# Performance work log

Hardware: AMD Instinct MI355X
Metric: run time of the kernel (lower is better)

The kernel has to match this reference:

```python
import jax, jax.numpy as jnp
import numpy as np

B, HW, N = 32, 4096, 16
E, KV, FFN = 256, 256, 1024
NUM_ITER = 3
EPS_LN = 1e-5
EPS_ATTN = 1e-5


def _ln(x, g, b):
    m = x.mean(-1, keepdims=True)
    v = ((x - m) ** 2).mean(-1, keepdims=True)
    return (x - m) / jnp.sqrt(v + EPS_LN) * g + b


def _gru_cell(x, h, w_ih, w_hh, b_ih, b_hh):
    # PyTorch GRUCell semantics; gate order r, z, n
    gi = x @ w_ih.T + b_ih
    gh = h @ w_hh.T + b_hh
    ir, iz, inn = jnp.split(gi, 3, axis=-1)
    hr, hz, hn = jnp.split(gh, 3, axis=-1)
    r = jax.nn.sigmoid(ir + hr)
    z = jax.nn.sigmoid(iz + hz)
    n = jnp.tanh(inn + r * hn)
    return (1.0 - z) * n + z * h


def setup_inputs() -> dict:
    key = jax.random.key(0)
    ks = jax.random.split(key, 16)
    s = 0.02
    return {
        "input": jax.random.normal(ks[0], (B, HW, KV), jnp.float32),
        "query": jax.random.normal(ks[1], (B, N, E), jnp.float32),
        "g_kv": jnp.ones((KV,), jnp.float32),
        "b_kv": jnp.zeros((KV,), jnp.float32),
        "w_k": jax.random.normal(ks[2], (E, KV), jnp.float32) * s,
        "w_v": jax.random.normal(ks[3], (E, KV), jnp.float32) * s,
        "g_q": jnp.ones((E,), jnp.float32),
        "b_q": jnp.zeros((E,), jnp.float32),
        "w_q": jax.random.normal(ks[4], (E, E), jnp.float32) * s,
        "w_ih": jax.random.normal(ks[5], (3 * E, E), jnp.float32) * s,
        "w_hh": jax.random.normal(ks[6], (3 * E, E), jnp.float32) * s,
        "b_ih": jnp.zeros((3 * E,), jnp.float32),
        "b_hh": jnp.zeros((3 * E,), jnp.float32),
        "g_2": jnp.ones((E,), jnp.float32),
        "b_2": jnp.zeros((E,), jnp.float32),
        "w_f1": jax.random.normal(ks[7], (FFN, E), jnp.float32) * s,
        "b_f1": jnp.zeros((FFN,), jnp.float32),
        "w_f2": jax.random.normal(ks[8], (E, FFN), jnp.float32) * s,
        "b_f2": jnp.zeros((E,), jnp.float32),
    }


def reference(input, query, g_kv, b_kv, w_k, w_v, g_q, b_q, w_q,
              w_ih, w_hh, b_ih, b_hh, g_2, b_2, w_f1, b_f1, w_f2, b_f2):
    b, n, e = query.shape
    kv = _ln(input, g_kv, b_kv)              # (b, hw, kv)
    k = kv @ w_k.T                           # (b, hw, e)
    v = kv @ w_v.T                           # (b, hw, e)
    scale = e ** (-0.5)

    q = query
    attn = None
    for i in range(NUM_ITER):
        if i + 1 == NUM_ITER:  # bi-level truncated backprop
            q = jax.lax.stop_gradient(q) + query - jax.lax.stop_gradient(query)
        slots_prev = q
        qn = _ln(q, g_q, b_q)
        qp = (qn @ w_q.T) * scale            # (b, n, e)
        logit = jnp.einsum("bqc,bkc->bqk", qp, k)
        attn = jax.nn.softmax(logit, axis=1)           # softmax over slots (inverted)
        attn_w = attn / (attn.sum(2, keepdims=True) + EPS_ATTN)
        updates = jnp.einsum("bqk,bkc->bqc", attn_w, v)
        slots = _gru_cell(updates.reshape(b * n, e), slots_prev.reshape(b * n, e),
                          w_ih, w_hh, b_ih, b_hh).reshape(b, n, e)
        h = jax.nn.gelu(_ln(slots, g_2, b_2) @ w_f1.T + b_f1)
        q = slots + h @ w_f2.T + b_f2
    return q, attn
```

## Files before the change

### kernel.cpp

```cpp
#include <hip/hip_runtime.h>
#include <math.h>

#define NB 32
#define HW 4096
#define NS 16
#define EDIM 256
#define FFND 1024
#define EPS_LN 1e-5f
#define EPS_ATTN 1e-5f
#define BPB 32
#define RPB 128
#define TROWS 16

__device__ __forceinline__ float sigmoidf_(float x) { return 1.0f / (1.0f + __expf(-x)); }
__device__ __forceinline__ float gelu_(float x) {
    float x3 = x * x * x;
    return 0.5f * x * (1.0f + tanhf(0.7978845608028654f * (x + 0.044715f * x3)));
}

__device__ __forceinline__ float rsum16(float v) {
    int x;
    x = __builtin_amdgcn_update_dpp(0, __float_as_int(v), 0x128, 0xF, 0xF, true);
    v += __int_as_float(x);
    x = __builtin_amdgcn_update_dpp(0, __float_as_int(v), 0x124, 0xF, 0xF, true);
    v += __int_as_float(x);
    x = __builtin_amdgcn_update_dpp(0, __float_as_int(v), 0x122, 0xF, 0xF, true);
    v += __int_as_float(x);
    x = __builtin_amdgcn_update_dpp(0, __float_as_int(v), 0x121, 0xF, 0xF, true);
    v += __int_as_float(x);
    return v;
}

__global__ void k_prep(const float* __restrict__ w_q, const float* __restrict__ w_k,
                       float* __restrict__ W) {
    const int j = blockIdx.x;
    const int c = threadIdx.x;
    float acc = 0.f;
    for (int e = 0; e < EDIM; ++e)
        acc += w_q[e * EDIM + j] * w_k[e * EDIM + c];
    W[j * EDIM + c] = acc * 0.0625f;
}

__global__ __launch_bounds__(256) void k_tr(const float* __restrict__ src,
                                            float* __restrict__ dst, int R, int C) {
    __shared__ float tile[64][65];
    const int tilesC = C >> 6;
    const int tR = (blockIdx.x / tilesC) << 6;
    const int tC = (blockIdx.x % tilesC) << 6;
    const int t = threadIdx.x;
    {
        const int r = t >> 2;
        const int c0 = (t & 3) << 4;
#pragma unroll
        for (int i = 0; i < 16; i += 4) {
            const float4 v = *reinterpret_cast<const float4*>(src + (size_t)(tR + r) * C + tC + c0 + i);
            tile[r][c0 + i] = v.x; tile[r][c0 + i + 1] = v.y;
            tile[r][c0 + i + 2] = v.z; tile[r][c0 + i + 3] = v.w;
        }
    }
    __syncthreads();
    {
        const int c = t >> 2;
        const int r0 = (t & 3) << 4;
#pragma unroll
        for (int i = 0; i < 16; ++i)
            dst[(size_t)(tC + c) * R + tR + r0 + i] = tile[r0 + i][c];
    }
}

__global__ void k_qproj(const float* __restrict__ qsrc, const float* __restrict__ g_q,
                        const float* __restrict__ b_q, const float* __restrict__ W,
                        const float* __restrict__ g_kv, const float* __restrict__ b_kv,
                        float* __restrict__ qpk, float* __restrict__ gqbq) {
    const int row = blockIdx.x;
    const int t = threadIdx.x;
    __shared__ float qn[EDIM];
    __shared__ float red[16];
    const float v = qsrc[(size_t)row * EDIM + t];
    float s = v, ss = v * v;
#pragma unroll
    for (int m = 1; m < 64; m <<= 1) { s += __shfl_xor(s, m); ss += __shfl_xor(ss, m); }
    const int wave = t >> 6, lane = t & 63;
    if (lane == 0) { red[wave] = s; red[8 + wave] = ss; }
    __syncthreads();
    const float st = red[0] + red[1] + red[2] + red[3];
    const float sst = red[8] + red[9] + red[10] + red[11];
    const float mean = st * (1.0f / EDIM);
    const float rstd = rsqrtf(sst * (1.0f / EDIM) - mean * mean + EPS_LN);
    qn[t] = (v - mean) * rstd * g_q[t] + b_q[t];
    __syncthreads();
    float acc = 0.f;
    for (int j = 0; j < EDIM; ++j)
        acc += qn[j] * W[j * EDIM + t];
    qpk[(size_t)row * EDIM + t] = acc;
    float u = acc * g_kv[t];
    float w2 = acc * b_kv[t];
#pragma unroll
    for (int m = 1; m < 64; m <<= 1) { u += __shfl_xor(u, m); w2 += __shfl_xor(w2, m); }
    __syncthreads();
    if (lane == 0) { red[wave] = u; red[8 + wave] = w2; }
    __syncthreads();
    if (t == 0) {
        const int b = row >> 4, sl = row & 15;
        gqbq[b * 32 + sl] = red[0] + red[1] + red[2] + red[3];
        gqbq[b * 32 + 16 + sl] = red[8] + red[9] + red[10] + red[11];
    }
}

template <bool LAST>
__global__ __launch_bounds__(256, 2) void k_bigpass(
    const float* __restrict__ input, const float* __restrict__ qpk,
    const float* __restrict__ gqbq, const float* __restrict__ g_kv,
    float* __restrict__ pacc, float* __restrict__ psum, float* __restrict__ attn_out) {
    const int b = blockIdx.x >> 5;
    const int sub = blockIdx.x & 31;
    const int t = threadIdx.x;
    const int w = t >> 6;
    const int lane = t & 63;
    const int g = t >> 4;
    const int j = t & 15;

    __shared__ __align__(16) float G[NS][EDIM];
    __shared__ __align__(16) float stage[TROWS][264];
    __shared__ __align__(16) float wrec[TROWS][20];
    __shared__ float gqbq_s[2][NS];

#pragma unroll
    for (int i = 0; i < 4; ++i) {
        const int idx = i * 1024 + t * 4;
        const float4 qv = *reinterpret_cast<const float4*>(qpk + (size_t)b * 4096 + idx);
        const float4 gv = *reinterpret_cast<const float4*>(g_kv + (idx & 255));
        *reinterpret_cast<float4*>(&G[0][0] + idx) =
            make_float4(qv.x * gv.x, qv.y * gv.y, qv.z * gv.z, qv.w * gv.w);
    }
    if (t < 32) gqbq_s[t >> 4][t & 15] = gqbq[b * 32 + t];
    __syncthreads();

    float acc[4][4];
    float S[4], A[4];
#pragma unroll
    for (int si = 0; si < 4; ++si) {
        acc[si][0] = acc[si][1] = acc[si][2] = acc[si][3] = 0.f;
        S[si] = 0.f; A[si] = 0.f;
    }

    const int rowbase = sub * RPB;
#pragma unroll 1
    for (int tt = 0; tt < RPB / TROWS; ++tt) {
        const int grow = rowbase + tt * TROWS + g;
        const float* xa = input + ((size_t)b * HW + grow) * EDIM;

        float p[NS];
#pragma unroll
        for (int s = 0; s < NS; ++s) p[s] = 0.f;
        float s1 = 0.f, s2 = 0.f;
#pragma unroll
        for (int c = 0; c < 4; ++c) {
            const int off = (c * 16 + j) * 4;
            const float4 x = *reinterpret_cast<const float4*>(xa + off);
            *reinterpret_cast<float4*>(&stage[g][off]) = x;
            s1 += x.x + x.y + x.z + x.w;
            s2 += x.x * x.x + x.y * x.y + x.z * x.z + x.w * x.w;
#pragma unroll
            for (int s = 0; s < NS; ++s) {
                const float4 gg = *reinterpret_cast<const float4*>(&G[s][off]);
                p[s] += x.x * gg.x + x.y * gg.y + x.z * gg.z + x.w * gg.w;
            }
        }
        s1 = rsum16(s1);
        s2 = rsum16(s2);
#pragma unroll
        for (int s = 0; s < NS; ++s) p[s] = rsum16(p[s]);

        const float mean = s1 * (1.0f / EDIM);
        const float rstd = rsqrtf(s2 * (1.0f / EDIM) - mean * mean + EPS_LN);
        float mx = -1e30f;
#pragma unroll
        for (int s = 0; s < NS; ++s) {
            p[s] = rstd * (p[s] - mean * gqbq_s[0][s]) + gqbq_s[1][s];
            mx = fmaxf(mx, p[s]);
        }
        float tot = 0.f;
#pragma unroll
        for (int s = 0; s < NS; ++s) { p[s] = __expf(p[s] - mx); tot += p[s]; }
        const float inv = 1.0f / tot;
#pragma unroll
        for (int s = 0; s < NS; ++s) p[s] *= inv;

        if (j == 0) {
#pragma unroll
            for (int sq = 0; sq < 4; ++sq)
                *reinterpret_cast<float4*>(&wrec[g][sq * 4]) =
                    make_float4(p[sq * 4], p[sq * 4 + 1], p[sq * 4 + 2], p[sq * 4 + 3]);
            wrec[g][16] = rstd;
            wrec[g][17] = rstd * mean;
            if (LAST) {
#pragma unroll
                for (int s = 0; s < NS; ++s)
                    attn_out[((size_t)(b * NS + s)) * HW + grow] = p[s];
            }
        }
        __syncthreads();

        {
            const int ch = lane * 4;
            const int sbase = w * 4;
#pragma unroll
            for (int r = 0; r < TROWS; ++r) {
                const float4 xv = *reinterpret_cast<const float4*>(&stage[r][ch]);
                const float4 at = *reinterpret_cast<const float4*>(&wrec[r][sbase]);
                const float rr = wrec[r][16];
                const float rm = wrec[r][17];
                float wg;
                wg = at.x * rr;
                acc[0][0] += wg * xv.x; acc[0][1] += wg * xv.y;
                acc[0][2] += wg * xv.z; acc[0][3] += wg * xv.w;
                S[0] += at.x; A[0] += at.x * rm;
                wg = at.y * rr;
                acc[1][0] += wg * xv.x; acc[1][1] += wg * xv.y;
                acc[1][2] += wg * xv.z; acc[1][3] += wg * xv.w;
                S[1] += at.y; A[1] += at.y * rm;
                wg = at.z * rr;
                acc[2][0] += wg * xv.x; acc[2][1] += wg * xv.y;
                acc[2][2] += wg * xv.z; acc[2][3] += wg * xv.w;
                S[2] += at.z; A[2] += at.z * rm;
                wg = at.w * rr;
                acc[3][0] += wg * xv.x; acc[3][1] += wg * xv.y;
                acc[3][2] += wg * xv.z; acc[3][3] += wg * xv.w;
                S[3] += at.w; A[3] += at.w * rm;
            }
        }
        __syncthreads();
    }

#pragma unroll
    for (int si = 0; si < 4; ++si) {
        *reinterpret_cast<float4*>(
            pacc + ((size_t)blockIdx.x * NS + w * 4 + si) * EDIM + lane * 4) =
            make_float4(acc[si][0], acc[si][1], acc[si][2], acc[si][3]);
    }
    if (lane == 0) {
#pragma unroll
        for (int si = 0; si < 4; ++si) {
            psum[blockIdx.x * 32 + w * 4 + si] = S[si];
            psum[blockIdx.x * 32 + 16 + w * 4 + si] = A[si];
        }
    }
}

__global__ __launch_bounds__(256) void k_upd(
    const float* __restrict__ pacc, const float* __restrict__ psum,
    const float* __restrict__ g_kv, const float* __restrict__ b_kv,
    const float* __restrict__ w_vT, float* __restrict__ updates) {
    const int rt = blockIdx.x >> 1;
    const int ct = blockIdx.x & 1;
    const int row0 = rt * 4;
    const int b = row0 >> 4;
    const int s0 = row0 & 15;
    const int t = threadIdx.x;
    __shared__ __align__(16) float ub[4][EDIM];
    __shared__ float sSA[4][2];

    if (t < 8) {
        const int r = t & 3;
        const int isA = t >> 2;
        float v = 0.f;
        for (int p = 0; p < BPB; ++p)
            v += psum[(b * BPB + p) * 32 + isA * 16 + s0 + r];
        sSA[r][isA] = v;
    }
    __syncthreads();
#pragma unroll
    for (int r = 0; r < 4; ++r) {
        float V = 0.f;
        for (int p = 0; p < BPB; ++p)
            V += pacc[((size_t)(b * BPB + p) * NS + s0 + r) * EDIM + t];
        const float Sv = sSA[r][0], Av = sSA[r][1];
        ub[r][t] = (g_kv[t] * (V - Av) + b_kv[t] * Sv) / (Sv + EPS_ATTN);
    }
    __syncthreads();

    const int c = ct * 128 + (t & 127);
    const int half = t >> 7;
    const float* u0 = ub[2 * half];
    const float* u1 = ub[2 * half + 1];
    float a0 = 0.f, a1 = 0.f;
#pragma unroll 4
    for (int j = 0; j < EDIM; j += 4) {
        const float4 x0 = *reinterpret_cast<const float4*>(u0 + j);
        const float4 x1 = *reinterpret_cast<const float4*>(u1 + j);
        const float w0 = w_vT[(size_t)j * EDIM + c];
        const float w1 = w_vT[(size_t)(j + 1) * EDIM + c];
        const float w2 = w_vT[(size_t)(j + 2) * EDIM + c];
        const float w3 = w_vT[(size_t)(j + 3) * EDIM + c];
        a0 += x0.x * w0 + x0.y * w1 + x0.z * w2 + x0.w * w3;
        a1 += x1.x * w0 + x1.y * w1 + x1.z * w2 + x1.w * w3;
    }
    updates[(size_t)(row0 + 2 * half) * EDIM + c] = a0;
    updates[(size_t)(row0 + 2 * half + 1) * EDIM + c] = a1;
}

__global__ __launch_bounds__(256) void k_gates(
    const float* __restrict__ updates, const float* __restrict__ qprev,
    const float* __restrict__ w_ihT, const float* __restrict__ w_hhT,
    const float* __restrict__ b_ih, const float* __restrict__ b_hh,
    float* __restrict__ gig) {
    const int rt = blockIdx.x / 6;
    const int ct = blockIdx.x % 6;
    const int row0 = rt * 4;
    const int t = threadIdx.x;
    const bool ih = ct < 3;
    const int lc = (ih ? ct : ct - 3) * 256 + t;
    const float* __restrict__ src = ih ? updates : qprev;
    const float* __restrict__ wT = ih ? w_ihT : w_hhT;

    __shared__ __align__(16) float in4[4][EDIM];
#pragma unroll
    for (int r = 0; r < 4; ++r)
        in4[r][t] = src[(size_t)(row0 + r) * EDIM + t];
    __syncthreads();

    float a0 = 0.f, a1 = 0.f, a2 = 0.f, a3 = 0.f;
#pragma unroll 4
    for (int j = 0; j < EDIM; j += 4) {
        const float4 x0 = *reinterpret_cast<const float4*>(&in4[0][j]);
        const float4 x1 = *reinterpret_cast<const float4*>(&in4[1][j]);
        const float4 x2 = *reinterpret_cast<const float4*>(&in4[2][j]);
        const float4 x3 = *reinterpret_cast<const float4*>(&in4[3][j]);
        const float w0 = wT[(size_t)j * 768 + lc];
        const float w1 = wT[(size_t)(j + 1) * 768 + lc];
        const float w2 = wT[(size_t)(j + 2) * 768 + lc];
        const float w3 = wT[(size_t)(j + 3) * 768 + lc];
        a0 += x0.x * w0 + x0.y * w1 + x0.z * w2 + x0.w * w3;
        a1 += x1.x * w0 + x1.y * w1 + x1.z * w2 + x1.w * w3;
        a2 += x2.x * w0 + x2.y * w1 + x2.z * w2 + x2.w * w3;
        a3 += x3.x * w0 + x3.y * w1 + x3.z * w2 + x3.w * w3;
    }
    const float bias = ih ? b_ih[lc] : b_hh[lc];
    const int gcol = ih ? lc : 768 + lc;
    gig[(size_t)(row0 + 0) * 1536 + gcol] = a0 + bias;
    gig[(size_t)(row0 + 1) * 1536 + gcol] = a1 + bias;
    gig[(size_t)(row0 + 2) * 1536 + gcol] = a2 + bias;
    gig[(size_t)(row0 + 3) * 1536 + gcol] = a3 + bias;
}

__global__ __launch_bounds__(256) void k_gruffn1(
    const float* __restrict__ gig, const float* __restrict__ qprev,
    const float* __restrict__ g_2, const float* __restrict__ b_2,
    const float* __restrict__ w_f1T, const float* __restrict__ b_f1,
    float* __restrict__ slots, float* __restrict__ h1) {
    const int rt = blockIdx.x >> 2;
    const int ct = blockIdx.x & 3;
    const int row0 = rt * 4;
    const int t = threadIdx.x;
    const int wave = t >> 6, lane = t & 63;
    __shared__ __align__(16) float ln2[4][EDIM];
    __shared__ float red[4][8];

    float sl[4];
#pragma unroll
    for (int r = 0; r < 4; ++r) {
        const size_t base = (size_t)(row0 + r) * 1536;
        const float ir = gig[base + t];
        const float iz = gig[base + 256 + t];
        const float inn = gig[base + 512 + t];
        const float hr = gig[base + 768 + t];
        const float hz = gig[base + 1024 + t];
        const float hn = gig[base + 1280 + t];
        const float h = qprev[(size_t)(row0 + r) * EDIM + t];
        const float rg = sigmoidf_(ir + hr);
        const float z = sigmoidf_(iz + hz);
        const float n = tanhf(inn + rg * hn);
        sl[r] = (1.0f - z) * n + z * h;
    }
    if (ct == 0) {
#pragma unroll
        for (int r = 0; r < 4; ++r)
            slots[(size_t)(row0 + r) * EDIM + t] = sl[r];
    }
    {
        float a[4], qq[4];
#pragma unroll
        for (int r = 0; r < 4; ++r) { a[r] = sl[r]; qq[r] = sl[r] * sl[r]; }
#pragma unroll
        for (int m = 1; m < 64; m <<= 1) {
#pragma unroll
            for (int r = 0; r < 4; ++r) {
                a[r] += __shfl_xor(a[r], m);
                qq[r] += __shfl_xor(qq[r], m);
            }
        }
        if (lane == 0) {
#pragma unroll
            for (int r = 0; r < 4; ++r) { red[wave][r] = a[r]; red[wave][4 + r] = qq[r]; }
        }
    }
    __syncthreads();
    {
        const float g = g_2[t], bb = b_2[t];
#pragma unroll
        for (int r = 0; r < 4; ++r) {
            const float Sv = red[0][r] + red[1][r] + red[2][r] + red[3][r];
            const float Qv = red[0][4 + r] + red[1][4 + r] + red[2][4 + r] + red[3][4 + r];
            const float mn = Sv * (1.0f / EDIM);
            const float rs = rsqrtf(Qv * (1.0f / EDIM) - mn * mn + EPS_LN);
            ln2[r][t] = (sl[r] - mn) * rs * g + bb;
        }
    }
    __syncthreads();

    const int c = ct * 256 + t;
    float a0 = 0.f, a1 = 0.f, a2 = 0.f, a3 = 0.f;
#pragma unroll 4
    for (int j = 0; j < EDIM; j += 4) {
        const float4 x0 = *reinterpret_cast<const float4*>(&ln2[0][j]);
        const float4 x1 = *reinterpret_cast<const float4*>(&ln2[1][j]);
        const float4 x2 = *reinterpret_cast<const float4*>(&ln2[2][j]);
        const float4 x3 = *reinterpret_cast<const float4*>(&ln2[3][j]);
        const float w0 = w_f1T[(size_t)j * FFND + c];
        const float w1 = w_f1T[(size_t)(j + 1) * FFND + c];
        const float w2 = w_f1T[(size_t)(j + 2) * FFND + c];
        const float w3 = w_f1T[(size_t)(j + 3) * FFND + c];
        a0 += x0.x * w0 + x0.y * w1 + x0.z * w2 + x0.w * w3;
        a1 += x1.x * w0 + x1.y * w1 + x1.z * w2 + x1.w * w3;
        a2 += x2.x * w0 + x2.y * w1 + x2.z * w2 + x2.w * w3;
        a3 += x3.x * w0 + x3.y * w1 + x3.z * w2 + x3.w * w3;
    }
    const float bf = b_f1[c];
    h1[(size_t)(row0 + 0) * FFND + c] = gelu_(a0 + bf);
    h1[(size_t)(row0 + 1) * FFND + c] = gelu_(a1 + bf);
    h1[(size_t)(row0 + 2) * FFND + c] = gelu_(a2 + bf);
    h1[(size_t)(row0 + 3) * FFND + c] = gelu_(a3 + bf);
}

__global__ __launch_bounds__(256) void k_ffn2qpk(
    const float* __restrict__ h1, const float* __restrict__ slots,
    const float* __restrict__ w_f2T, const float* __restrict__ b_f2,
    const float* __restrict__ query,
    const float* __restrict__ g_q, const float* __restrict__ b_q,
    const float* __restrict__ W,
    const float* __restrict__ g_kv, const float* __restrict__ b_kv,
    float* __restrict__ q_out, float* __restrict__ qpk, float* __restrict__ gqbq,
    int adjust, int do_qpk) {
    const int row0 = blockIdx.x * 2;
    const int t = threadIdx.x;
    const int wave = t >> 6, lane = t & 63;
    __shared__ __align__(16) float in2[2][FFND];
    __shared__ float red[4][4];
    __shared__ __align__(16) float qn[2][EDIM];

#pragma unroll
    for (int r = 0; r < 2; ++r)
        *reinterpret_cast<float4*>(&in2[r][t * 4]) =
            *reinterpret_cast<const float4*>(h1 + (size_t)(row0 + r) * FFND + t * 4);
    __syncthreads();
    float a0 = 0.f, a1 = 0.f;
#pragma unroll 4
    for (int j = 0; j < FFND; j += 4) {
        const float4 x0 = *reinterpret_cast<const float4*>(&in2[0][j]);
        const float4 x1 = *reinterpret_cast<const float4*>(&in2[1][j]);
        const float w0 = w_f2T[(size_t)j * EDIM + t];
        const float w1 = w_f2T[(size_t)(j + 1) * EDIM + t];
        const float w2 = w_f2T[(size_t)(j + 2) * EDIM + t];
        const float w3 = w_f2T[(size_t)(j + 3) * EDIM + t];
        a0 += x0.x * w0 + x0.y * w1 + x0.z * w2 + x0.w * w3;
        a1 += x1.x * w0 + x1.y * w1 + x1.z * w2 + x1.w * w3;
    }
    const float bf = b_f2[t];
    float v0 = slots[(size_t)row0 * EDIM + t] + a0 + bf;
    float v1 = slots[(size_t)(row0 + 1) * EDIM + t] + a1 + bf;
    if (adjust) {
        const float qq0 = query[(size_t)row0 * EDIM + t];
        const float qq1 = query[(size_t)(row0 + 1) * EDIM + t];
        v0 = (v0 + qq0) - qq0;
        v1 = (v1 + qq1) - qq1;
    }
    q_out[(size_t)row0 * EDIM + t] = v0;
    q_out[(size_t)(row0 + 1) * EDIM + t] = v1;

    if (!do_qpk) return;

    {
        float a0r = v0, q0 = v0 * v0, a1r = v1, q1 = v1 * v1;
#pragma unroll
        for (int m = 1; m < 64; m <<= 1) {
            a0r += __shfl_xor(a0r, m); q0 += __shfl_xor(q0, m);
            a1r += __shfl_xor(a1r, m); q1 += __shfl_xor(q1, m);
        }
        if (lane == 0) { red[wave][0] = a0r; red[wave][1] = q0; red[wave][2] = a1r; red[wave][3] = q1; }
    }
    __syncthreads();
    {
        const float S0 = red[0][0] + red[1][0] + red[2][0] + red[3][0];
        const float Q0 = red[0][1] + red[1][1] + red[2][1] + red[3][1];
        const float S1 = red[0][2] + red[1][2] + red[2][2] + red[3][2];
        const float Q1 = red[0][3] + red[1][3] + red[2][3] + red[3][3];
        const float m0 = S0 * (1.0f / EDIM);
        const float r0 = rsqrtf(Q0 * (1.0f / EDIM) - m0 * m0 + EPS_LN);
        const float m1 = S1 * (1.0f / EDIM);
        const float r1 = rsqrtf(Q1 * (1.0f / EDIM) - m1 * m1 + EPS_LN);
        const float g = g_q[t], bb = b_q[t];
        qn[0][t] = (v0 - m0) * r0 * g + bb;
        qn[1][t] = (v1 - m1) * r1 * g + bb;
    }
    __syncthreads();
    float p0 = 0.f, p1 = 0.f;
#pragma unroll 4
    for (int j = 0; j < EDIM; j += 4) {
        const float4 x0 = *reinterpret_cast<const float4*>(&qn[0][j]);
        const float4 x1 = *reinterpret_cast<const float4*>(&qn[1][j]);
        const float w0 = W[(size_t)j * EDIM + t];
        const float w1 = W[(size_t)(j + 1) * EDIM + t];
        const float w2 = W[(size_t)(j + 2) * EDIM + t];
        const float w3 = W[(size_t)(j + 3) * EDIM + t];
        p0 += x0.x * w0 + x0.y * w1 + x0.z * w2 + x0.w * w3;
        p1 += x1.x * w0 + x1.y * w1 + x1.z * w2 + x1.w * w3;
    }
    qpk[(size_t)row0 * EDIM + t] = p0;
    qpk[(size_t)(row0 + 1) * EDIM + t] = p1;
    {
        const float gk = g_kv[t], bk = b_kv[t];
        float u0 = p0 * gk, w0 = p0 * bk, u1 = p1 * gk, w1 = p1 * bk;
#pragma unroll
        for (int m = 1; m < 64; m <<= 1) {
            u0 += __shfl_xor(u0, m); w0 += __shfl_xor(w0, m);
            u1 += __shfl_xor(u1, m); w1 += __shfl_xor(w1, m);
        }
        __syncthreads();
        if (lane == 0) { red[wave][0] = u0; red[wave][1] = w0; red[wave][2] = u1; red[wave][3] = w1; }
        __syncthreads();
        if (t == 0) {
            const int b = row0 >> 4;
            const int sl = row0 & 15;
            gqbq[b * 32 + sl] = red[0][0] + red[1][0] + red[2][0] + red[3][0];
            gqbq[b * 32 + 16 + sl] = red[0][1] + red[1][1] + red[2][1] + red[3][1];
            gqbq[b * 32 + sl + 1] = red[0][2] + red[1][2] + red[2][2] + red[3][2];
            gqbq[b * 32 + 16 + sl + 1] = red[0][3] + red[1][3] + red[2][3] + red[3][3];
        }
    }
}

extern "C" void kernel_launch(void* const* d_in, const int* in_sizes, int n_in,
                              void* d_out, int out_size, void* d_ws, size_t ws_size,
                              hipStream_t stream) {
    const float* input = (const float*)d_in[0];
    const float* query = (const float*)d_in[1];
    const float* g_kv = (const float*)d_in[2];
    const float* b_kv = (const float*)d_in[3];
    const float* w_k = (const float*)d_in[4];
    const float* w_v = (const float*)d_in[5];
    const float* g_q = (const float*)d_in[6];
    const float* b_q = (const float*)d_in[7];
    const float* w_q = (const float*)d_in[8];
    const float* w_ih = (const float*)d_in[9];
    const float* w_hh = (const float*)d_in[10];
    const float* b_ih = (const float*)d_in[11];
    const float* b_hh = (const float*)d_in[12];
    const float* g_2 = (const float*)d_in[13];
    const float* b_2 = (const float*)d_in[14];
    const float* w_f1 = (const float*)d_in[15];
    const float* b_f1 = (const float*)d_in[16];
    const float* w_f2 = (const float*)d_in[17];
    const float* b_f2 = (const float*)d_in[18];

    float* ws = (float*)d_ws;
    float* W = ws;        ws += 65536;
    float* qpk = ws;      ws += 131072;
    float* gqbq = ws;     ws += 1024;
    float* psum = ws;     ws += 32768;
    float* q_ws = ws;     ws += 131072;
    float* updates = ws;  ws += 131072;
    float* slots = ws;    ws += 131072;
    float* w_vT = ws;     ws += 65536;
    float* w_ihT = ws;    ws += 196608;
    float* w_hhT = ws;    ws += 196608;
    float* w_f1T = ws;    ws += 262144;
    float* w_f2T = ws;    ws += 262144;
    float* pacc = ws;     ws += (size_t)NB * BPB * NS * EDIM;
    float* gig = pacc;
    float* h1 = pacc + 786432;

    float* out_q = (float*)d_out;
    float* out_attn = out_q + (size_t)NB * NS * EDIM;

    k_prep<<<256, 256, 0, stream>>>(w_q, w_k, W);
    k_tr<<<16, 256, 0, stream>>>(w_v, w_vT, 256, 256);
    k_tr<<<48, 256, 0, stream>>>(w_ih, w_ihT, 768, 256);
    k_tr<<<48, 256, 0, stream>>>(w_hh, w_hhT, 768, 256);
    k_tr<<<64, 256, 0, stream>>>(w_f1, w_f1T, 1024, 256);
    k_tr<<<64, 256, 0, stream>>>(w_f2, w_f2T, 256, 1024);
    k_qproj<<<512, 256, 0, stream>>>(query, g_q, b_q, W, g_kv, b_kv, qpk, gqbq);

    const float* qprev[3] = {query, q_ws, q_ws};
    float* qdst[3] = {q_ws, q_ws, out_q};
    const int adj[3] = {0, 1, 0};

    for (int it = 0; it < 3; ++it) {
        const bool last = (it == 2);
        if (last)
            k_bigpass<true><<<NB * BPB, 256, 0, stream>>>(input, qpk, gqbq, g_kv, pacc, psum, out_attn);
        else
            k_bigpass<false><<<NB * BPB, 256, 0, stream>>>(input, qpk, gqbq, g_kv, pacc, psum, nullptr);
        k_upd<<<256, 256, 0, stream>>>(pacc, psum, g_kv, b_kv, w_vT, updates);
        k_gates<<<768, 256, 0, stream>>>(updates, qprev[it], w_ihT, w_hhT, b_ih, b_hh, gig);
        k_gruffn1<<<512, 256, 0, stream>>>(gig, qprev[it], g_2, b_2, w_f1T, b_f1, slots, h1);
        k_ffn2qpk<<<256, 256, 0, stream>>>(h1, slots, w_f2T, b_f2, query, g_q, b_q, W,
                                           g_kv, b_kv, qdst[it], qpk, gqbq,
                                           adj[it], last ? 0 : 1);
    }
}
```

Before: 495.7 us.

## Hold slot projections in registers and split logit work across waves

Each wave now keeps four slots' worth of the gamma-scaled query-key projection in registers instead of reading all 16 slots from shared memory for every row. The logit computation is split so each wave handles 4 slots across the staged rows, with results written to a small LDS table. The softmax over slots then runs with one slot per lane using DPP max and sum reductions, and the attention output is written by all 16 lanes rather than by one. This reduces LDS traffic and the per-thread 16-way reduction work, but adds two barriers per tile and 64 extra registers per thread for Greg, which may hurt occupancy under the 2-blocks launch bound.

```diff
diff --git a/kernel.cpp b/kernel.cpp
--- a/kernel.cpp
+++ b/kernel.cpp
@@ -30,6 +30,18 @@
     v += __int_as_float(x);
     return v;
 }
+__device__ __forceinline__ float rmax16(float v) {
+    int x;
+    x = __builtin_amdgcn_update_dpp(0, __float_as_int(v), 0x128, 0xF, 0xF, true);
+    v = fmaxf(v, __int_as_float(x));
+    x = __builtin_amdgcn_update_dpp(0, __float_as_int(v), 0x124, 0xF, 0xF, true);
+    v = fmaxf(v, __int_as_float(x));
+    x = __builtin_amdgcn_update_dpp(0, __float_as_int(v), 0x122, 0xF, 0xF, true);
+    v = fmaxf(v, __int_as_float(x));
+    x = __builtin_amdgcn_update_dpp(0, __float_as_int(v), 0x121, 0xF, 0xF, true);
+    v = fmaxf(v, __int_as_float(x));
+    return v;
+}
 
 __global__ void k_prep(const float* __restrict__ w_q, const float* __restrict__ w_k,
                        float* __restrict__ W) {
@@ -117,24 +129,29 @@
     const int t = threadIdx.x;
     const int w = t >> 6;
     const int lane = t & 63;
+    const int gp = (t >> 4) & 3;
     const int g = t >> 4;
     const int j = t & 15;
 
-    __shared__ __align__(16) float G[NS][EDIM];
     __shared__ __align__(16) float stage[TROWS][264];
     __shared__ __align__(16) float wrec[TROWS][20];
-    __shared__ float gqbq_s[2][NS];
-
-#pragma unroll
-    for (int i = 0; i < 4; ++i) {
-        const int idx = i * 1024 + t * 4;
-        const float4 qv = *reinterpret_cast<const float4*>(qpk + (size_t)b * 4096 + idx);
-        const float4 gv = *reinterpret_cast<const float4*>(g_kv + (idx & 255));
-        *reinterpret_cast<float4*>(&G[0][0] + idx) =
-            make_float4(qv.x * gv.x, qv.y * gv.y, qv.z * gv.z, qv.w * gv.w);
-    }
-    if (t < 32) gqbq_s[t >> 4][t & 15] = gqbq[b * 32 + t];
-    __syncthreads();
+    __shared__ __align__(16) float logit_lds[TROWS][NS];
+
+    const float gqj = gqbq[b * 32 + j];
+    const float bqj = gqbq[b * 32 + 16 + j];
+
+    float4 Greg[4][4];
+#pragma unroll
+    for (int sp = 0; sp < 4; ++sp) {
+#pragma unroll
+        for (int c = 0; c < 4; ++c) {
+            const int off = (c * 16 + j) * 4;
+            const float4 qv = *reinterpret_cast<const float4*>(
+                qpk + (size_t)b * 4096 + (w * 4 + sp) * 256 + off);
+            const float4 gv = *reinterpret_cast<const float4*>(g_kv + off);
+            Greg[sp][c] = make_float4(qv.x * gv.x, qv.y * gv.y, qv.z * gv.z, qv.w * gv.w);
+        }
+    }
 
     float acc[4][4];
     float S[4], A[4];
@@ -150,9 +167,6 @@
         const int grow = rowbase + tt * TROWS + g;
         const float* xa = input + ((size_t)b * HW + grow) * EDIM;
 
-        float p[NS];
-#pragma unroll
-        for (int s = 0; s < NS; ++s) p[s] = 0.f;
         float s1 = 0.f, s2 = 0.f;
 #pragma unroll
         for (int c = 0; c < 4; ++c) {
@@ -161,44 +175,47 @@
             *reinterpret_cast<float4*>(&stage[g][off]) = x;
             s1 += x.x + x.y + x.z + x.w;
             s2 += x.x * x.x + x.y * x.y + x.z * x.z + x.w * x.w;
-#pragma unroll
-            for (int s = 0; s < NS; ++s) {
-                const float4 gg = *reinterpret_cast<const float4*>(&G[s][off]);
-                p[s] += x.x * gg.x + x.y * gg.y + x.z * gg.z + x.w * gg.w;
-            }
         }
         s1 = rsum16(s1);
         s2 = rsum16(s2);
-#pragma unroll
-        for (int s = 0; s < NS; ++s) p[s] = rsum16(p[s]);
-
         const float mean = s1 * (1.0f / EDIM);
         const float rstd = rsqrtf(s2 * (1.0f / EDIM) - mean * mean + EPS_LN);
-        float mx = -1e30f;
-#pragma unroll
-        for (int s = 0; s < NS; ++s) {
-            p[s] = rstd * (p[s] - mean * gqbq_s[0][s]) + gqbq_s[1][s];
-            mx = fmaxf(mx, p[s]);
-        }
-        float tot = 0.f;
-#pragma unroll
-        for (int s = 0; s < NS; ++s) { p[s] = __expf(p[s] - mx); tot += p[s]; }
-        const float inv = 1.0f / tot;
-#pragma unroll
-        for (int s = 0; s < NS; ++s) p[s] *= inv;
-
-        if (j == 0) {
-#pragma unroll
-            for (int sq = 0; sq < 4; ++sq)
-                *reinterpret_cast<float4*>(&wrec[g][sq * 4]) =
-                    make_float4(p[sq * 4], p[sq * 4 + 1], p[sq * 4 + 2], p[sq * 4 + 3]);
-            wrec[g][16] = rstd;
-            wrec[g][17] = rstd * mean;
-            if (LAST) {
-#pragma unroll
-                for (int s = 0; s < NS; ++s)
-                    attn_out[((size_t)(b * NS + s)) * HW + grow] = p[s];
+        __syncthreads();
+
+#pragma unroll
+        for (int rb = 0; rb < 4; ++rb) {
+            const int row = rb * 4 + gp;
+            float d0 = 0.f, d1 = 0.f, d2 = 0.f, d3 = 0.f;
+#pragma unroll
+            for (int c = 0; c < 4; ++c) {
+                const int off = (c * 16 + j) * 4;
+                const float4 x = *reinterpret_cast<const float4*>(&stage[row][off]);
+                d0 += x.x * Greg[0][c].x + x.y * Greg[0][c].y + x.z * Greg[0][c].z + x.w * Greg[0][c].w;
+                d1 += x.x * Greg[1][c].x + x.y * Greg[1][c].y + x.z * Greg[1][c].z + x.w * Greg[1][c].w;
+                d2 += x.x * Greg[2][c].x + x.y * Greg[2][c].y + x.z * Greg[2][c].z + x.w * Greg[2][c].w;
+                d3 += x.x * Greg[3][c].x + x.y * Greg[3][c].y + x.z * Greg[3][c].z + x.w * Greg[3][c].w;
             }
+            d0 = rsum16(d0); d1 = rsum16(d1); d2 = rsum16(d2); d3 = rsum16(d3);
+            if (j == 0)
+                *reinterpret_cast<float4*>(&logit_lds[row][w * 4]) =
+                    make_float4(d0, d1, d2, d3);
+        }
+        __syncthreads();
+
+        {
+            float L = logit_lds[g][j];
+            L = rstd * (L - mean * gqj) + bqj;
+            const float mx = rmax16(L);
+            const float p = __expf(L - mx);
+            const float tot = rsum16(p);
+            const float at = p / tot;
+            wrec[g][j] = at;
+            if (j == 0) {
+                wrec[g][16] = rstd;
+                wrec[g][17] = rstd * mean;
+            }
+            if (LAST)
+                attn_out[((size_t)(b * NS + j)) * HW + grow] = at;
         }
         __syncthreads();
 
```

After: 475.6 us. 1.04x faster.
